# Optimization experiments

Hardware: AMD Instinct MI355X
Metric: run time of the kernel (lower is better)

## Reference

```python
import jax, jax.numpy as jnp
import numpy as np

SEQ_LENGTH = 1000
NUM_FEATURES = 5
HIDDEN = 128


def setup_inputs() -> dict:
    key = jax.random.key(0)
    ks = jax.random.split(key, 12)
    k = 1.0 / np.sqrt(HIDDEN)  # torch default uniform bound
    # recurrence stays numerically bounded; math is identical.
    u = lambda kk, shape, s=k: jax.random.uniform(kk, shape, jnp.float32, -s, s)
    return {
        "x": jax.random.normal(ks[0], (256, 800, NUM_FEATURES), jnp.float32),
        "h_state": jnp.zeros((2, 256, HIDDEN), jnp.float32),
        "w_ih0": u(ks[1], (HIDDEN, NUM_FEATURES)),
        "w_hh0": u(ks[2], (HIDDEN, HIDDEN), 0.5 * k),
        "b_ih0": u(ks[3], (HIDDEN,)),
        "b_hh0": u(ks[4], (HIDDEN,)),
        "w_ih1": u(ks[5], (HIDDEN, HIDDEN), 0.5 * k),
        "w_hh1": u(ks[6], (HIDDEN, HIDDEN), 0.5 * k),
        "b_ih1": u(ks[7], (HIDDEN,)),
        "b_hh1": u(ks[8], (HIDDEN,)),
        "w_out": u(ks[9], (1, HIDDEN)),
        "b_out": u(ks[10], (1,)),
    }


def reference(x, h_state, w_ih0, w_hh0, b_ih0, b_hh0,
              w_ih1, w_hh1, b_ih1, b_hh1, w_out, b_out):
    B, T_in, F = x.shape
    # pad time dim to SEQ_LENGTH with zeros (torch.cat with delta)
    pad = jnp.zeros((B, SEQ_LENGTH - T_in, F), x.dtype)
    xp = jnp.concatenate([x, pad], axis=1)  # [B, 1000, F]
    xs = jnp.swapaxes(xp, 0, 1)  # [T, B, F] for scan

    def step(carry, x_t):
        h0, h1 = carry
        h0 = jax.nn.relu(x_t @ w_ih0.T + b_ih0 + h0 @ w_hh0.T + b_hh0)
        h1 = jax.nn.relu(h0 @ w_ih1.T + b_ih1 + h1 @ w_hh1.T + b_hh1)
        return (h0, h1), h1

    (h0f, h1f), ys = jax.lax.scan(step, (h_state[0], h_state[1]), xs)
    r_out = jnp.swapaxes(ys, 0, 1)  # [B, 1000, H]
    out = jax.nn.sigmoid(r_out @ w_out.T + b_out)  # [B, 1000, 1]
    return out[:, :T_in], jnp.stack([h0f, h1f])
```

## Files before the change

kernel.cpp:

```cpp
#include <hip/hip_runtime.h>
#include <math.h>


#define TT    1000
#define TIN   800
#define HD    128
#define NF    5
#define BATCH 256
#define RS    136
#define AS    132
#define SK1   20
#define NSTEP (TT + SK1)

typedef _Float16 h16x2 __attribute__((ext_vector_type(2)));
typedef _Float16 h16x8 __attribute__((ext_vector_type(8)));
typedef float    f32x4 __attribute__((ext_vector_type(4)));

template<int CTRL>
__device__ __forceinline__ float dpp_mov(float v) {
    union { float f; int i; } u, r;
    u.f = v;
    r.i = __builtin_amdgcn_update_dpp(0, u.i, CTRL, 0xF, 0xF, true);
    return r.f;
}

__global__ __launch_bounds__(384, 1) void rnn_c6(
    const float* __restrict__ x,
    const float* __restrict__ h_state,
    const float* __restrict__ w_ih0,
    const float* __restrict__ w_hh0,
    const float* __restrict__ b_ih0,
    const float* __restrict__ b_hh0,
    const float* __restrict__ w_ih1,
    const float* __restrict__ w_hh1,
    const float* __restrict__ b_ih1,
    const float* __restrict__ b_hh1,
    const float* __restrict__ w_out,
    const float* __restrict__ b_out,
    float* __restrict__ out)
{
    __shared__ __align__(16) _Float16 x_h[TIN * 8];
    __shared__ __align__(16) _Float16 ring0[32][RS];
    __shared__ __align__(16) _Float16 ring1[32][RS];
    __shared__ __align__(16) float    A_f[32][AS];
    __shared__ __align__(16) float    xc_f[32][AS];
    __shared__ float y_lds[TIN];

    const int tid  = threadIdx.x;
    const int bb   = blockIdx.x;
    const int wv   = tid >> 6;
    const int lane = tid & 63;

    for (int i = tid; i < TIN * 8; i += 384) x_h[i] = (_Float16)0.f;
    __syncthreads();
    for (int i = tid; i < TIN * NF; i += 384) {
        int t = i / 5, f = i - 5 * t;
        x_h[t * 8 + f] = (_Float16)x[bb * (TIN * NF) + i];
    }
    if (tid < HD) {
        ring0[31][tid] = (_Float16)h_state[bb * HD + tid];
        ring1[31][tid] = (_Float16)h_state[BATCH * HD + bb * HD + tid];
    }

    const int c    = lane & 3;
    const int rg   = lane >> 2;
    const int g    = 2 * (c & 1) + ((c >> 1) & 1);
    const int half = wv & 1;
    const int row  = half * 64 + rg * 4 + g;

    union WU {
        h16x2 wp[4][16];
        h16x8 af[4][4];
    } W;
    h16x2 wo[16];
    h16x2 xwa[3], xwb[3];
    float bias = 0.f;

    if (wv < 4) {
        const float* Wsrc = (wv < 2) ? w_hh0 : w_hh1;
        #pragma unroll
        for (int j = 0; j < 4; ++j) {
            const float* rp = Wsrc + (half * 64 + rg * 4 + (j ^ g)) * HD + c * 32;
            #pragma unroll
            for (int t = 0; t < 16; ++t) {
                h16x2 w2 = { (_Float16)rp[2 * t], (_Float16)rp[2 * t + 1] };
                W.wp[j][t] = w2;
            }
        }
        bias = (wv < 2) ? (b_ih0[row] + b_hh0[row])
                        : (b_ih1[row] + b_hh1[row]);
    } else {
        const int m0 = (wv == 4) ? 0 : 64;
        #pragma unroll
        for (int mt = 0; mt < 4; ++mt) {
            #pragma unroll
            for (int kt = 0; kt < 4; ++kt) {
                const float* rp = w_ih1 + (m0 + mt * 16 + (lane & 15)) * HD
                                + kt * 32 + (lane >> 4) * 8;
                h16x8 v;
                #pragma unroll
                for (int j = 0; j < 8; ++j) v[j] = (_Float16)rp[j];
                W.af[mt][kt] = v;
            }
        }
        if (wv == 4) {
            const int c4 = lane & 3;
            #pragma unroll
            for (int t = 0; t < 16; ++t) {
                h16x2 w2 = { (_Float16)w_out[c4 * 32 + 2 * t],
                             (_Float16)w_out[c4 * 32 + 2 * t + 1] };
                wo[t] = w2;
            }
        } else {
            #pragma unroll
            for (int k = 0; k < 3; ++k) {
                _Float16 a0 = (_Float16)w_ih0[(2 * lane) * NF + 2 * k];
                _Float16 a1 = (2 * k + 1 < NF) ? (_Float16)w_ih0[(2 * lane) * NF + 2 * k + 1] : (_Float16)0.f;
                _Float16 b0 = (_Float16)w_ih0[(2 * lane + 1) * NF + 2 * k];
                _Float16 b1 = (2 * k + 1 < NF) ? (_Float16)w_ih0[(2 * lane + 1) * NF + 2 * k + 1] : (_Float16)0.f;
                h16x2 wa = { a0, a1 }; xwa[k] = wa;
                h16x2 wb = { b0, b1 }; xwb[k] = wb;
            }
        }
    }
    const float bout = b_out[0];

    float hfin = 0.f;

    __syncthreads();

    auto xc_burst = [&](int tb) {
        #pragma unroll
        for (int ti = 0; ti < 16; ++ti) {
            const int t = tb + ti;
            h16x8 xv = *(const h16x8*)(&x_h[t * 8]);
            h16x2 xp0 = { xv[0], xv[1] };
            h16x2 xp1 = { xv[2], xv[3] };
            h16x2 xp2 = { xv[4], xv[5] };
            float c0 = __builtin_amdgcn_fdot2(xwa[2], xp2, 0.f, false);
            c0 = __builtin_amdgcn_fdot2(xwa[1], xp1, c0, false);
            c0 = __builtin_amdgcn_fdot2(xwa[0], xp0, c0, false);
            float c1 = __builtin_amdgcn_fdot2(xwb[2], xp2, 0.f, false);
            c1 = __builtin_amdgcn_fdot2(xwb[1], xp1, c1, false);
            c1 = __builtin_amdgcn_fdot2(xwb[0], xp0, c1, false);
            *(float2*)(&xc_f[t & 31][2 * lane]) = make_float2(c0, c1);
        }
    };

    if (wv == 5) xc_burst(0);
    __syncthreads();

    auto matvec = [&](const _Float16* base) -> float {
        h16x8 hv[4];
        #pragma unroll
        for (int u2 = 0; u2 < 4; ++u2)
            hv[u2] = *(const h16x8*)(base + c * 32 + 8 * u2);
        float a[4] = {0.f, 0.f, 0.f, 0.f};
        #pragma unroll
        for (int j = 0; j < 4; ++j) {
            float aj = 0.f;
            #pragma unroll
            for (int t = 0; t < 16; ++t) {
                h16x2 hp = { hv[t >> 2][2 * (t & 3)], hv[t >> 2][2 * (t & 3) + 1] };
                aj = __builtin_amdgcn_fdot2(W.wp[j][t], hp, aj, false);
            }
            a[j] = aj;
        }
        a[0] += dpp_mov<0xB1>(a[2]);
        a[1] += dpp_mov<0xB1>(a[3]);
        a[0] += dpp_mov<0x4E>(a[1]);
        return a[0];
    };

    for (int s = 0; s < NSTEP; ++s) {
        if (wv < 2) {
            if (s < TT) {
                float v = matvec(&ring0[(s + 31) & 31][0]) + bias;
                if (s < TIN) v += xc_f[s & 31][row];
                v = fmaxf(v, 0.f);
                ring0[s & 31][row] = (_Float16)v;
                if (s == TT - 1) hfin = v;
            }
        } else if (wv < 4) {
            if (s >= SK1) {
                const int u = s - SK1;
                float v = matvec(&ring1[(u + 31) & 31][0]);
                v = fmaxf(v + bias + A_f[u & 31][row], 0.f);
                ring1[u & 31][row] = (_Float16)v;
                if (u == TT - 1) hfin = v;
            }
        } else {
            if (s >= 17 && s <= 1009 && ((s - 17) & 15) == 0) {
                const int m0 = (wv == 4) ? 0 : 64;
                const int ub = s - 17;
                const int un = ub + (lane & 15);
                h16x8 bf[4];
                #pragma unroll
                for (int kt = 0; kt < 4; ++kt)
                    bf[kt] = *(const h16x8*)(&ring0[un & 31]
                                             [kt * 32 + (lane >> 4) * 8]);
                #pragma unroll
                for (int mt = 0; mt < 4; ++mt) {
                    f32x4 acc = {0.f, 0.f, 0.f, 0.f};
                    #pragma unroll
                    for (int kt = 0; kt < 4; ++kt)
                        acc = __builtin_amdgcn_mfma_f32_16x16x32_f16(
                            W.af[mt][kt], bf[kt], acc, 0, 0, 0);
                    if (un < TT)
                        *(f32x4*)(&A_f[un & 31]
                                  [m0 + mt * 16 + (lane >> 4) * 4]) = acc;
                }
            }
            if (wv == 4) {
                if (s >= 37 && s <= 821 && ((s - 37) & 15) == 0) {
                    const int slot = lane >> 2;
                    const int c4   = lane & 3;
                    const int t    = (s - 37) + slot;
                    const _Float16* rb = &ring1[t & 31][0] + c4 * 32;
                    float z = 0.f;
                    #pragma unroll
                    for (int u2 = 0; u2 < 4; ++u2) {
                        h16x8 hv = *(const h16x8*)(rb + 8 * u2);
                        h16x2 hp0 = { hv[0], hv[1] };
                        h16x2 hp1 = { hv[2], hv[3] };
                        h16x2 hp2 = { hv[4], hv[5] };
                        h16x2 hp3 = { hv[6], hv[7] };
                        z = __builtin_amdgcn_fdot2(wo[4 * u2 + 0], hp0, z, false);
                        z = __builtin_amdgcn_fdot2(wo[4 * u2 + 1], hp1, z, false);
                        z = __builtin_amdgcn_fdot2(wo[4 * u2 + 2], hp2, z, false);
                        z = __builtin_amdgcn_fdot2(wo[4 * u2 + 3], hp3, z, false);
                    }
                    z += dpp_mov<0xB1>(z);
                    z += dpp_mov<0x4E>(z);
                    if (c4 == 0) y_lds[t] = 1.f / (1.f + expf(-(z + bout)));
                }
            } else {
                if (s >= 9 && s <= 777 && ((s - 9) & 15) == 0) {
                    xc_burst(s + 7);
                }
            }
        }
        __syncthreads();
    }

    for (int i = tid; i < TIN; i += 384)
        out[bb * TIN + i] = y_lds[i];
    if (wv < 2)
        out[TIN * BATCH + bb * HD + row] = hfin;
    else if (wv < 4)
        out[TIN * BATCH + BATCH * HD + bb * HD + row] = hfin;
}

extern "C" void kernel_launch(void* const* d_in, const int* in_sizes, int n_in,
                              void* d_out, int out_size, void* d_ws, size_t ws_size,
                              hipStream_t stream) {
    (void)in_sizes; (void)n_in; (void)d_ws; (void)ws_size; (void)out_size;
    rnn_c6<<<dim3(BATCH), dim3(384), 0, stream>>>(
        (const float*)d_in[0],  (const float*)d_in[1],
        (const float*)d_in[2],  (const float*)d_in[3],
        (const float*)d_in[4],  (const float*)d_in[5],
        (const float*)d_in[6],  (const float*)d_in[7],
        (const float*)d_in[8],  (const float*)d_in[9],
        (const float*)d_in[10], (const float*)d_in[11],
        (float*)d_out);
}
```

Before: 428.8 us.

## Keep recurrent state in registers, rotate via DPP, sync every eight steps

Each recurrence layer now runs in a single wave. The hidden state stays in registers, and the 128x128 matvec is done by rotating h across lanes with DPP, swizzle and bpermute instead of reading it back from LDS each step. Block barriers drop from once per step to once every eight steps, relying on ring buffers and a slightly larger layer-1 skew (SK1=24) for slack between producer and consumer waves. Launch bounds allow two blocks per CU. The risk is heavier per-wave serial dot-product chains and subtle cross-wave LDS races caused by the reduced synchronisation.

```diff
diff --git a/kernel.cpp b/kernel.cpp
--- a/kernel.cpp
+++ b/kernel.cpp
@@ -9,8 +9,8 @@
 #define BATCH 256
 #define RS    136
 #define AS    132
-#define SK1   20
-#define NSTEP (TT + SK1)
+#define SK1   24
+#define NSTEP 1024
 
 typedef _Float16 h16x2 __attribute__((ext_vector_type(2)));
 typedef _Float16 h16x8 __attribute__((ext_vector_type(8)));
@@ -23,8 +23,27 @@
     r.i = __builtin_amdgcn_update_dpp(0, u.i, CTRL, 0xF, 0xF, true);
     return r.f;
 }
-
-__global__ __launch_bounds__(384, 1) void rnn_c6(
+__device__ __forceinline__ int h2i(h16x2 v) { union { h16x2 h; int i; } u; u.h = v; return u.i; }
+__device__ __forceinline__ h16x2 i2h(int v) { union { h16x2 h; int i; } u; u.i = v; return u.h; }
+template<int CTRL>
+__device__ __forceinline__ h16x2 dpp_h2(h16x2 v) {
+    return i2h(__builtin_amdgcn_update_dpp(0, h2i(v), CTRL, 0xF, 0xF, true));
+}
+
+#define TICK(x, r) \
+    a0 = __builtin_amdgcn_fdot2(W.wp[x][r][0], cur, a0, false); \
+    a1 = __builtin_amdgcn_fdot2(W.wp[x][r][1], cur, a1, false);
+#define RING16(x, V) { h16x2 cur = (V); float a0 = 0.f, a1 = 0.f; \
+    TICK(x,0)  cur = dpp_h2<0xB1>(cur);  TICK(x,1)  cur = dpp_h2<0x1B>(cur);  \
+    TICK(x,2)  cur = dpp_h2<0xB1>(cur);  TICK(x,3)  cur = dpp_h2<0x141>(cur); \
+    TICK(x,4)  cur = dpp_h2<0xB1>(cur);  TICK(x,5)  cur = dpp_h2<0x1B>(cur);  \
+    TICK(x,6)  cur = dpp_h2<0xB1>(cur);  TICK(x,7)  cur = dpp_h2<0x140>(cur); \
+    TICK(x,8)  cur = dpp_h2<0xB1>(cur);  TICK(x,9)  cur = dpp_h2<0x1B>(cur);  \
+    TICK(x,10) cur = dpp_h2<0xB1>(cur);  TICK(x,11) cur = dpp_h2<0x141>(cur); \
+    TICK(x,12) cur = dpp_h2<0xB1>(cur);  TICK(x,13) cur = dpp_h2<0x1B>(cur);  \
+    TICK(x,14) cur = dpp_h2<0xB1>(cur);  TICK(x,15) t0 += a0; t1 += a1; }
+
+__global__ __launch_bounds__(384, 2) void rnn_rr(
     const float* __restrict__ x,
     const float* __restrict__ h_state,
     const float* __restrict__ w_ih0,
@@ -50,6 +69,8 @@
     const int bb   = blockIdx.x;
     const int wv   = tid >> 6;
     const int lane = tid & 63;
+    const int R    = lane >> 4;
+    const int p    = lane & 15;
 
     for (int i = tid; i < TIN * 8; i += 384) x_h[i] = (_Float16)0.f;
     __syncthreads();
@@ -57,40 +78,44 @@
         int t = i / 5, f = i - 5 * t;
         x_h[t * 8 + f] = (_Float16)x[bb * (TIN * NF) + i];
     }
-    if (tid < HD) {
-        ring0[31][tid] = (_Float16)h_state[bb * HD + tid];
-        ring1[31][tid] = (_Float16)h_state[BATCH * HD + bb * HD + tid];
-    }
-
-    const int c    = lane & 3;
-    const int rg   = lane >> 2;
-    const int g    = 2 * (c & 1) + ((c >> 1) & 1);
-    const int half = wv & 1;
-    const int row  = half * 64 + rg * 4 + g;
 
     union WU {
-        h16x2 wp[4][16];
+        h16x2 wp[4][16][2];
         h16x8 af[4][4];
     } W;
     h16x2 wo[16];
     h16x2 xwa[3], xwb[3];
-    float bias = 0.f;
-
-    if (wv < 4) {
-        const float* Wsrc = (wv < 2) ? w_hh0 : w_hh1;
-        #pragma unroll
-        for (int j = 0; j < 4; ++j) {
-            const float* rp = Wsrc + (half * 64 + rg * 4 + (j ^ g)) * HD + c * 32;
+    float bias0 = 0.f, bias1 = 0.f;
+    h16x2 hc = { (_Float16)0.f, (_Float16)0.f };
+
+    if (wv < 2) {
+        const float* Wsrc = (wv == 0) ? w_hh0 : w_hh1;
+        #pragma unroll
+        for (int xx = 0; xx < 4; ++xx) {
             #pragma unroll
-            for (int t = 0; t < 16; ++t) {
-                h16x2 w2 = { (_Float16)rp[2 * t], (_Float16)rp[2 * t + 1] };
-                W.wp[j][t] = w2;
-            }
-        }
-        bias = (wv < 2) ? (b_ih0[row] + b_hh0[row])
-                        : (b_ih1[row] + b_hh1[row]);
-    } else {
-        const int m0 = (wv == 4) ? 0 : 64;
+            for (int r = 0; r < 16; ++r) {
+                const int q = 16 * (R ^ xx) + (p ^ r);
+                const float* c0 = Wsrc + (2 * lane) * HD + 2 * q;
+                const float* c1 = Wsrc + (2 * lane + 1) * HD + 2 * q;
+                h16x2 w0 = { (_Float16)c0[0], (_Float16)c0[1] };
+                h16x2 w1 = { (_Float16)c1[0], (_Float16)c1[1] };
+                W.wp[xx][r][0] = w0;
+                W.wp[xx][r][1] = w1;
+            }
+        }
+        if (wv == 0) {
+            bias0 = b_ih0[2 * lane] + b_hh0[2 * lane];
+            bias1 = b_ih0[2 * lane + 1] + b_hh0[2 * lane + 1];
+            hc[0] = (_Float16)h_state[bb * HD + 2 * lane];
+            hc[1] = (_Float16)h_state[bb * HD + 2 * lane + 1];
+        } else {
+            bias0 = b_ih1[2 * lane] + b_hh1[2 * lane];
+            bias1 = b_ih1[2 * lane + 1] + b_hh1[2 * lane + 1];
+            hc[0] = (_Float16)h_state[BATCH * HD + bb * HD + 2 * lane];
+            hc[1] = (_Float16)h_state[BATCH * HD + bb * HD + 2 * lane + 1];
+        }
+    } else if (wv < 4) {
+        const int m0 = (wv == 2) ? 0 : 64;
         #pragma unroll
         for (int mt = 0; mt < 4; ++mt) {
             #pragma unroll
@@ -103,31 +128,30 @@
                 W.af[mt][kt] = v;
             }
         }
-        if (wv == 4) {
-            const int c4 = lane & 3;
-            #pragma unroll
-            for (int t = 0; t < 16; ++t) {
-                h16x2 w2 = { (_Float16)w_out[c4 * 32 + 2 * t],
-                             (_Float16)w_out[c4 * 32 + 2 * t + 1] };
-                wo[t] = w2;
-            }
-        } else {
-            #pragma unroll
-            for (int k = 0; k < 3; ++k) {
-                _Float16 a0 = (_Float16)w_ih0[(2 * lane) * NF + 2 * k];
-                _Float16 a1 = (2 * k + 1 < NF) ? (_Float16)w_ih0[(2 * lane) * NF + 2 * k + 1] : (_Float16)0.f;
-                _Float16 b0 = (_Float16)w_ih0[(2 * lane + 1) * NF + 2 * k];
-                _Float16 b1 = (2 * k + 1 < NF) ? (_Float16)w_ih0[(2 * lane + 1) * NF + 2 * k + 1] : (_Float16)0.f;
-                h16x2 wa = { a0, a1 }; xwa[k] = wa;
-                h16x2 wb = { b0, b1 }; xwb[k] = wb;
-            }
+    } else if (wv == 4) {
+        const int c4 = lane & 3;
+        #pragma unroll
+        for (int t = 0; t < 16; ++t) {
+            h16x2 w2 = { (_Float16)w_out[c4 * 32 + 2 * t],
+                         (_Float16)w_out[c4 * 32 + 2 * t + 1] };
+            wo[t] = w2;
+        }
+    } else {
+        #pragma unroll
+        for (int k = 0; k < 3; ++k) {
+            _Float16 a0 = (_Float16)w_ih0[(2 * lane) * NF + 2 * k];
+            _Float16 a1 = (2 * k + 1 < NF) ? (_Float16)w_ih0[(2 * lane) * NF + 2 * k + 1] : (_Float16)0.f;
+            _Float16 b0 = (_Float16)w_ih0[(2 * lane + 1) * NF + 2 * k];
+            _Float16 b1 = (2 * k + 1 < NF) ? (_Float16)w_ih0[(2 * lane + 1) * NF + 2 * k + 1] : (_Float16)0.f;
+            h16x2 wa = { a0, a1 }; xwa[k] = wa;
+            h16x2 wb = { b0, b1 }; xwb[k] = wb;
         }
     }
     const float bout = b_out[0];
-
-    float hfin = 0.f;
-
-    __syncthreads();
+    const int a32 = (lane ^ 32) << 2;
+    const int a48 = (lane ^ 48) << 2;
+
+    float hfin0 = 0.f, hfin1 = 0.f;
 
     auto xc_burst = [&](int tb) {
         #pragma unroll
@@ -147,51 +171,52 @@
         }
     };
 
+    __syncthreads();
     if (wv == 5) xc_burst(0);
     __syncthreads();
 
-    auto matvec = [&](const _Float16* base) -> float {
-        h16x8 hv[4];
-        #pragma unroll
-        for (int u2 = 0; u2 < 4; ++u2)
-            hv[u2] = *(const h16x8*)(base + c * 32 + 8 * u2);
-        float a[4] = {0.f, 0.f, 0.f, 0.f};
-        #pragma unroll
-        for (int j = 0; j < 4; ++j) {
-            float aj = 0.f;
-            #pragma unroll
-            for (int t = 0; t < 16; ++t) {
-                h16x2 hp = { hv[t >> 2][2 * (t & 3)], hv[t >> 2][2 * (t & 3) + 1] };
-                aj = __builtin_amdgcn_fdot2(W.wp[j][t], hp, aj, false);
-            }
-            a[j] = aj;
-        }
-        a[0] += dpp_mov<0xB1>(a[2]);
-        a[1] += dpp_mov<0xB1>(a[3]);
-        a[0] += dpp_mov<0x4E>(a[1]);
-        return a[0];
+    auto matrot = [&](h16x2 hin, float& t0, float& t1) {
+        const int hb = h2i(hin);
+        h16x2 vB = i2h(__builtin_amdgcn_ds_swizzle(hb, 0x401F));
+        h16x2 vC = i2h(__builtin_amdgcn_ds_bpermute(a32, hb));
+        h16x2 vD = i2h(__builtin_amdgcn_ds_bpermute(a48, hb));
+        t0 = 0.f; t1 = 0.f;
+        RING16(0, hin)
+        RING16(1, vB)
+        RING16(2, vC)
+        RING16(3, vD)
     };
 
     for (int s = 0; s < NSTEP; ++s) {
-        if (wv < 2) {
+        if (wv == 0) {
             if (s < TT) {
-                float v = matvec(&ring0[(s + 31) & 31][0]) + bias;
-                if (s < TIN) v += xc_f[s & 31][row];
-                v = fmaxf(v, 0.f);
-                ring0[s & 31][row] = (_Float16)v;
-                if (s == TT - 1) hfin = v;
-            }
-        } else if (wv < 4) {
+                float2 xcv = make_float2(0.f, 0.f);
+                if (s < TIN) xcv = *(const float2*)(&xc_f[s & 31][2 * lane]);
+                float t0, t1;
+                matrot(hc, t0, t1);
+                float v0 = fmaxf(t0 + bias0 + xcv.x, 0.f);
+                float v1 = fmaxf(t1 + bias1 + xcv.y, 0.f);
+                h16x2 nh = { (_Float16)v0, (_Float16)v1 };
+                hc = nh;
+                *(h16x2*)(&ring0[s & 31][2 * lane]) = nh;
+                if (s == TT - 1) { hfin0 = v0; hfin1 = v1; }
+            }
+        } else if (wv == 1) {
             if (s >= SK1) {
                 const int u = s - SK1;
-                float v = matvec(&ring1[(u + 31) & 31][0]);
-                v = fmaxf(v + bias + A_f[u & 31][row], 0.f);
-                ring1[u & 31][row] = (_Float16)v;
-                if (u == TT - 1) hfin = v;
-            }
-        } else {
+                float2 av = *(const float2*)(&A_f[u & 31][2 * lane]);
+                float t0, t1;
+                matrot(hc, t0, t1);
+                float v0 = fmaxf(t0 + bias0 + av.x, 0.f);
+                float v1 = fmaxf(t1 + bias1 + av.y, 0.f);
+                h16x2 nh = { (_Float16)v0, (_Float16)v1 };
+                hc = nh;
+                *(h16x2*)(&ring1[u & 31][2 * lane]) = nh;
+                if (u == TT - 1) { hfin0 = v0; hfin1 = v1; }
+            }
+        } else if (wv < 4) {
             if (s >= 17 && s <= 1009 && ((s - 17) & 15) == 0) {
-                const int m0 = (wv == 4) ? 0 : 64;
+                const int m0 = (wv == 2) ? 0 : 64;
                 const int ub = s - 17;
                 const int un = ub + (lane & 15);
                 h16x8 bf[4];
@@ -211,51 +236,50 @@
                                   [m0 + mt * 16 + (lane >> 4) * 4]) = acc;
                 }
             }
-            if (wv == 4) {
-                if (s >= 37 && s <= 821 && ((s - 37) & 15) == 0) {
-                    const int slot = lane >> 2;
-                    const int c4   = lane & 3;
-                    const int t    = (s - 37) + slot;
-                    const _Float16* rb = &ring1[t & 31][0] + c4 * 32;
-                    float z = 0.f;
-                    #pragma unroll
-                    for (int u2 = 0; u2 < 4; ++u2) {
-                        h16x8 hv = *(const h16x8*)(rb + 8 * u2);
-                        h16x2 hp0 = { hv[0], hv[1] };
-                        h16x2 hp1 = { hv[2], hv[3] };
-                        h16x2 hp2 = { hv[4], hv[5] };
-                        h16x2 hp3 = { hv[6], hv[7] };
-                        z = __builtin_amdgcn_fdot2(wo[4 * u2 + 0], hp0, z, false);
-                        z = __builtin_amdgcn_fdot2(wo[4 * u2 + 1], hp1, z, false);
-                        z = __builtin_amdgcn_fdot2(wo[4 * u2 + 2], hp2, z, false);
-                        z = __builtin_amdgcn_fdot2(wo[4 * u2 + 3], hp3, z, false);
-                    }
-                    z += dpp_mov<0xB1>(z);
-                    z += dpp_mov<0x4E>(z);
-                    if (c4 == 0) y_lds[t] = 1.f / (1.f + expf(-(z + bout)));
+        } else if (wv == 4) {
+            if (s >= 41 && s <= 825 && ((s - 41) & 15) == 0) {
+                const int slot = lane >> 2;
+                const int c4   = lane & 3;
+                const int t    = (s - 41) + slot;
+                const _Float16* rb = &ring1[t & 31][0] + c4 * 32;
+                float z = 0.f;
+                #pragma unroll
+                for (int u2 = 0; u2 < 4; ++u2) {
+                    h16x8 hv = *(const h16x8*)(rb + 8 * u2);
+                    h16x2 hp0 = { hv[0], hv[1] };
+                    h16x2 hp1 = { hv[2], hv[3] };
+                    h16x2 hp2 = { hv[4], hv[5] };
+                    h16x2 hp3 = { hv[6], hv[7] };
+                    z = __builtin_amdgcn_fdot2(wo[4 * u2 + 0], hp0, z, false);
+                    z = __builtin_amdgcn_fdot2(wo[4 * u2 + 1], hp1, z, false);
+                    z = __builtin_amdgcn_fdot2(wo[4 * u2 + 2], hp2, z, false);
+                    z = __builtin_amdgcn_fdot2(wo[4 * u2 + 3], hp3, z, false);
                 }
-            } else {
-                if (s >= 9 && s <= 777 && ((s - 9) & 15) == 0) {
-                    xc_burst(s + 7);
-                }
-            }
-        }
-        __syncthreads();
+                z += dpp_mov<0xB1>(z);
+                z += dpp_mov<0x4E>(z);
+                if (c4 == 0) y_lds[t] = 1.f / (1.f + expf(-(z + bout)));
+            }
+        } else {
+            if (s >= 9 && s <= 777 && ((s - 9) & 15) == 0) {
+                xc_burst(s + 7);
+            }
+        }
+        if ((s & 7) == 7) __syncthreads();
     }
 
     for (int i = tid; i < TIN; i += 384)
         out[bb * TIN + i] = y_lds[i];
-    if (wv < 2)
-        out[TIN * BATCH + bb * HD + row] = hfin;
-    else if (wv < 4)
-        out[TIN * BATCH + BATCH * HD + bb * HD + row] = hfin;
+    if (wv == 0)
+        *(float2*)(&out[TIN * BATCH + bb * HD + 2 * lane]) = make_float2(hfin0, hfin1);
+    else if (wv == 1)
+        *(float2*)(&out[TIN * BATCH + BATCH * HD + bb * HD + 2 * lane]) = make_float2(hfin0, hfin1);
 }
 
 extern "C" void kernel_launch(void* const* d_in, const int* in_sizes, int n_in,
                               void* d_out, int out_size, void* d_ws, size_t ws_size,
                               hipStream_t stream) {
     (void)in_sizes; (void)n_in; (void)d_ws; (void)ws_size; (void)out_size;
-    rnn_c6<<<dim3(BATCH), dim3(384), 0, stream>>>(
+    rnn_rr<<<dim3(BATCH), dim3(384), 0, stream>>>(
         (const float*)d_in[0],  (const float*)d_in[1],
         (const float*)d_in[2],  (const float*)d_in[3],
         (const float*)d_in[4],  (const float*)d_in[5],
```

New measurement: 605.9 us. 1.41x slower.
